# Kernel optimization log

Measured on AMD Instinct MI355X. Metric: run time of the kernel, lower is better.

The kernel has to match this reference:

```python
import jax, jax.numpy as jnp
import numpy as np

H = 16
DH = 64  # n_state // n_head = 1024 // 16
EPS = 1e-6


def phi(x):
    return jax.nn.silu(x) + 1.0


def setup_inputs() -> dict:
    key = jax.random.key(0)
    ks = jax.random.split(key, 9)
    B, C, Tq, Tk = 8, 1024, 1500, 1500
    s = 1.0 / np.sqrt(C).astype(np.float32)
    return {
        "x": jax.random.normal(ks[0], (B, C, Tq, 1), jnp.float32),
        "xa": jax.random.normal(ks[1], (B, C, Tk, 1), jnp.float32),
        "Wq": jax.random.normal(ks[2], (C, C), jnp.float32) * s,
        "bq": jax.random.normal(ks[3], (C,), jnp.float32) * s,
        "Wk": jax.random.normal(ks[4], (C, C), jnp.float32) * s,
        "Wv": jax.random.normal(ks[5], (C, C), jnp.float32) * s,
        "bv": jax.random.normal(ks[6], (C,), jnp.float32) * s,
        "Wo": jax.random.normal(ks[7], (C, C), jnp.float32) * s,
        "bo": jax.random.normal(ks[8], (C,), jnp.float32) * s,
    }


def reference(x, xa, Wq, bq, Wk, Wv, bv, Wo, bo):
    # x: (B,C,Tq,1), xa: (B,C,Tk,1). 1x1 conv2d == matmul over channel dim.
    xq = x[..., 0]   # (B,C,Tq)
    xk = xa[..., 0]  # (B,C,Tk)
    q = jnp.einsum('oc,bct->bot', Wq, xq) + bq[None, :, None]
    k = jnp.einsum('oc,bct->bot', Wk, xk)  # key has no bias
    v = jnp.einsum('oc,bct->bot', Wv, xk) + bv[None, :, None]

    B, C, Tq = q.shape
    Tk = k.shape[2]
    pq = phi(q).reshape(B, H, DH, Tq)
    pk = phi(k).reshape(B, H, DH, Tk)
    vv = v.reshape(B, H, DH, Tk)

    k_sum = pk.sum(axis=3)            # (B,H,Dh) : sum_t phi(k)
    kv_sum = (pk * vv).sum(axis=3)    # (B,H,Dh) : diagonal phi(k)*v sum (as in source)
    den = jnp.einsum('bhdt,bhd->bht', pq, k_sum) + EPS  # (B,H,Tq)

    out = pq * kv_sum[..., None] / den[:, :, None, :]   # (B,H,Dh,Tq)
    out = out.reshape(B, C, Tq) / jnp.sqrt(jnp.asarray(DH, out.dtype))
    y = jnp.einsum('oc,bct->bot', Wo, out) + bo[None, :, None]
    return y[..., None]  # (B,C,Tq,1)
```

## Files before the change

### kernel.cpp

```cpp
#include <hip/hip_runtime.h>

typedef __attribute__((ext_vector_type(4))) float  f32x4;
typedef __attribute__((ext_vector_type(4))) float  float4v;
typedef __attribute__((ext_vector_type(8))) short  short8;
typedef __attribute__((ext_vector_type(4))) short  short4v;

#define TQ 1500
#define TP 1536
#define CC 1024
#define EPS 1e-6f

#define XT_OFF    ((size_t)0)
#define XAT_OFF   ((size_t)25165824)
#define OUT_OFF   ((size_t)50331648)
#define WB_OFF    ((size_t)75497472)
#define KSUM_OFF  ((size_t)83886080)
#define KVSUM_OFF ((size_t)83918848)

#define VMCNT4() asm volatile("s_waitcnt vmcnt(4)" ::: "memory")
#define VMCNT0() asm volatile("s_waitcnt vmcnt(0)" ::: "memory")
#define LGKM0()  asm volatile("s_waitcnt lgkmcnt(0)" ::: "memory")
#define SBAR()   __builtin_amdgcn_s_barrier()
#define SCHED0() __builtin_amdgcn_sched_barrier(0)

__device__ __forceinline__ float bf2f(short s) {
    union { unsigned u; float f; } v; v.u = ((unsigned)(unsigned short)s) << 16; return v.f;
}
__device__ __forceinline__ short f2bf(float f) {
    union { float f; unsigned u; } v; v.f = f;
    unsigned r = (v.u + 0x7FFFu + ((v.u >> 16) & 1u)) >> 16;
    return (short)r;
}
__device__ __forceinline__ float phi_f(float x) {
    return x / (1.f + __expf(-x)) + 1.f;
}
__device__ __forceinline__ void gl_lds16(const void* g, void* l) {
    __builtin_amdgcn_global_load_lds((const __attribute__((address_space(1))) void*)g,
                                     (__attribute__((address_space(3))) void*)l, 16, 0, 0);
}


__global__ __launch_bounds__(256)
void conv_w_kernel(const float* __restrict__ w0, const float* __restrict__ w1,
                   const float* __restrict__ w2, const float* __restrict__ w3,
                   short* __restrict__ o0, short* __restrict__ o1,
                   short* __restrict__ o2, short* __restrict__ o3)
{
    const int i = (blockIdx.x * 256 + threadIdx.x) * 4;
    float4v a = *(const float4v*)(w0 + i);
    float4v b = *(const float4v*)(w1 + i);
    float4v c = *(const float4v*)(w2 + i);
    float4v d = *(const float4v*)(w3 + i);
    short4v ra, rb, rc, rd;
#pragma unroll
    for (int j = 0; j < 4; ++j) {
        ra[j] = f2bf(a[j]); rb[j] = f2bf(b[j]); rc[j] = f2bf(c[j]); rd[j] = f2bf(d[j]);
    }
    *(short4v*)(o0 + i) = ra;
    *(short4v*)(o1 + i) = rb;
    *(short4v*)(o2 + i) = rc;
    *(short4v*)(o3 + i) = rd;
}

__global__ __launch_bounds__(256)
void xpose_kernel(const float* __restrict__ x, const float* __restrict__ xa,
                  short* __restrict__ xT, short* __restrict__ xaT)
{
    __shared__ float tile[64][65];
    const int z  = blockIdx.z;
    const int b  = z & 7;
    const float* src = (z < 8) ? x : xa;
    short* dst       = (z < 8) ? xT : xaT;
    const int c0 = blockIdx.y * 64;
    const int t0 = blockIdx.x * 64;
    const int tl = threadIdx.x & 63;
    const int q  = threadIdx.x >> 6;
    const int t  = t0 + tl;
#pragma unroll
    for (int i = 0; i < 16; ++i) {
        const int cl = q * 16 + i;
        float v = 0.f;
        if (t < TQ) v = src[((size_t)b * CC + c0 + cl) * TQ + t];
        tile[cl][tl] = v;
    }
    __syncthreads();
#pragma unroll
    for (int i = 0; i < 16; ++i) {
        const int t2 = q * 16 + i;
        dst[((size_t)b * TP + t0 + t2) * CC + c0 + tl] = f2bf(tile[tl][t2]);
    }
}


__global__ __launch_bounds__(256, 4)
void gemm_q_out_kernel(const short* __restrict__ xT, const short* __restrict__ Wqb,
                       const float* __restrict__ bq, const float* __restrict__ ksum,
                       const float* __restrict__ kvsum, short* __restrict__ outT)
{
    __shared__ short lds[3][8192];
    const int f    = blockIdx.x;
    const int L    = (f & 7) * 96 + (f >> 3);
    const int nt   = L % 8;
    const int mrow = L / 8;
    const int b    = mrow / 12;
    const int tid  = threadIdx.x;
    const int wave = tid >> 6, lane = tid & 63;
    const int wr = wave >> 1;
    const int wc = wave & 1;
    const int rl = lane & 15;
    const int q4 = lane >> 4;
    const int rg = (q4 ^ ((rl >> 1) & 3)) << 3;

    const int lrow = lane >> 2;
    const int kc   = ((lane & 3) ^ ((lrow >> 1) & 3)) << 3;
    const int row0 = wave * 32 + lrow;
    const short* aP0 = xT  + (size_t)(mrow * 128 + row0) * CC + kc;
    const short* aP1 = aP0 + 16 * CC;
    const short* bP0 = Wqb + (size_t)(nt * 128 + row0) * CC + kc;
    const short* bP1 = bP0 + 16 * CC;
    const int aD0 = wave * 1024, aD1 = aD0 + 512;
    const int bD0 = 4096 + aD0,  bD1 = bD0 + 512;

    const int aoff0 = (wr * 64 + rl) * 32 + rg;
    const int boff0 = 4096 + (wc * 64 + rl) * 32 + rg;

    f32x4 acc[4][4] = {};

#pragma unroll
    for (int s = 0; s < 2; ++s) {
        gl_lds16(aP0, &lds[s][aD0]); gl_lds16(aP1, &lds[s][aD1]);
        gl_lds16(bP0, &lds[s][bD0]); gl_lds16(bP1, &lds[s][bD1]);
        aP0 += 32; aP1 += 32; bP0 += 32; bP1 += 32;
    }
    VMCNT4(); SBAR();

    int cur = 0;
#pragma unroll 1
    for (int kt = 0; kt < 32; ++kt) {
        if (kt <= 29) {
            const int pn = (cur == 0) ? 2 : cur - 1;
            gl_lds16(aP0, &lds[pn][aD0]); gl_lds16(aP1, &lds[pn][aD1]);
            gl_lds16(bP0, &lds[pn][bD0]); gl_lds16(bP1, &lds[pn][bD1]);
            aP0 += 32; aP1 += 32; bP0 += 32; bP1 += 32;
        }
        short8 ra[4], rb[4];
#pragma unroll
        for (int i = 0; i < 4; ++i) {
            ra[i] = *(const short8*)&lds[cur][aoff0 + i * 512];
            rb[i] = *(const short8*)&lds[cur][boff0 + i * 512];
        }
        LGKM0(); SCHED0();
        __builtin_amdgcn_s_setprio(1);
#pragma unroll
        for (int i = 0; i < 4; ++i)
#pragma unroll
            for (int j = 0; j < 4; ++j)
                acc[i][j] = __builtin_amdgcn_mfma_f32_16x16x32_bf16(ra[i], rb[j], acc[i][j], 0, 0, 0);
        __builtin_amdgcn_s_setprio(0);
        if (kt <= 29)      { VMCNT4(); }
        else if (kt == 30) { VMCNT0(); }
        if (kt < 31) SBAR();
        cur = (cur == 2) ? 0 : cur + 1;
    }

    float bias[4], ks[4], kv[4];
#pragma unroll
    for (int j = 0; j < 4; ++j) {
        const int c = nt * 128 + wc * 64 + j * 16 + rl;
        bias[j] = bq[c];
        ks[j]   = ksum[b * CC + c];
        kv[j]   = kvsum[b * CC + c];
    }
#pragma unroll
    for (int i = 0; i < 4; ++i)
#pragma unroll
        for (int j = 0; j < 4; ++j)
#pragma unroll
            for (int r = 0; r < 4; ++r)
                acc[i][j][r] = phi_f(acc[i][j][r] + bias[j]);
#pragma unroll
    for (int i = 0; i < 4; ++i) {
#pragma unroll
        for (int r = 0; r < 4; ++r) {
            float d = acc[i][0][r] * ks[0] + acc[i][1][r] * ks[1]
                    + acc[i][2][r] * ks[2] + acc[i][3][r] * ks[3];
            d += __shfl_xor(d, 1); d += __shfl_xor(d, 2);
            d += __shfl_xor(d, 4); d += __shfl_xor(d, 8);
            const float inv = 0.125f / (d + EPS);
            const int trow = mrow * 128 + wr * 64 + i * 16 + q4 * 4 + r;
#pragma unroll
            for (int j = 0; j < 4; ++j) {
                const int c = nt * 128 + wc * 64 + j * 16 + rl;
                outT[(size_t)trow * CC + c] = f2bf(acc[i][j][r] * kv[j] * inv);
            }
        }
    }
}

__global__ __launch_bounds__(256, 4)
void gemm_kv_kernel(const short* __restrict__ xaT, const short* __restrict__ Wkb,
                    const short* __restrict__ Wvb, const float* __restrict__ bv,
                    float* __restrict__ ksum, float* __restrict__ kvsum)
{
    __shared__ short lds[3][8192];
    const int f    = blockIdx.x;
    const int L    = (f & 7) * 192 + (f >> 3);
    const int cb   = L % 16;
    const int mrow = L / 16;
    const int b    = mrow / 12;
    const int tid  = threadIdx.x;
    const int wave = tid >> 6, lane = tid & 63;
    const int wr = wave >> 1;
    const int wc = wave & 1;
    const int rl = lane & 15;
    const int q4 = lane >> 4;
    const int rg = (q4 ^ ((rl >> 1) & 3)) << 3;

    const int lrow = lane >> 2;
    const int kc   = ((lane & 3) ^ ((lrow >> 1) & 3)) << 3;
    const int row0 = wave * 32 + lrow;
    const short* aP0 = xaT + (size_t)(mrow * 128 + row0) * CC + kc;
    const short* aP1 = aP0 + 16 * CC;
    const short* bPanel = (wave < 2)
        ? Wkb + (size_t)cb * 64 * CC
        : Wvb + (size_t)cb * 64 * CC - (size_t)64 * CC;
    const short* bP0 = bPanel + (size_t)row0 * CC + kc;
    const short* bP1 = bP0 + 16 * CC;
    const int aD0 = wave * 1024, aD1 = aD0 + 512;
    const int bD0 = 4096 + aD0,  bD1 = bD0 + 512;

    const int aoff0 = (wr * 64 + rl) * 32 + rg;
    const int boffK = 4096 + (wc * 32 + rl) * 32 + rg;
    const int boffV = boffK + 2048;

    f32x4 acc[4][4] = {};

#pragma unroll
    for (int s = 0; s < 2; ++s) {
        gl_lds16(aP0, &lds[s][aD0]); gl_lds16(aP1, &lds[s][aD1]);
        gl_lds16(bP0, &lds[s][bD0]); gl_lds16(bP1, &lds[s][bD1]);
        aP0 += 32; aP1 += 32; bP0 += 32; bP1 += 32;
    }
    VMCNT4(); SBAR();

    int cur = 0;
#pragma unroll 1
    for (int kt = 0; kt < 32; ++kt) {
        if (kt <= 29) {
            const int pn = (cur == 0) ? 2 : cur - 1;
            gl_lds16(aP0, &lds[pn][aD0]); gl_lds16(aP1, &lds[pn][aD1]);
            gl_lds16(bP0, &lds[pn][bD0]); gl_lds16(bP1, &lds[pn][bD1]);
            aP0 += 32; aP1 += 32; bP0 += 32; bP1 += 32;
        }
        short8 ra[4], rb[4];
#pragma unroll
        for (int i = 0; i < 4; ++i)
            ra[i] = *(const short8*)&lds[cur][aoff0 + i * 512];
#pragma unroll
        for (int j = 0; j < 2; ++j) {
            rb[j]     = *(const short8*)&lds[cur][boffK + j * 512];
            rb[j + 2] = *(const short8*)&lds[cur][boffV + j * 512];
        }
        LGKM0(); SCHED0();
        __builtin_amdgcn_s_setprio(1);
#pragma unroll
        for (int i = 0; i < 4; ++i)
#pragma unroll
            for (int j = 0; j < 4; ++j)
                acc[i][j] = __builtin_amdgcn_mfma_f32_16x16x32_bf16(ra[i], rb[j], acc[i][j], 0, 0, 0);
        __builtin_amdgcn_s_setprio(0);
        if (kt <= 29)      { VMCNT4(); }
        else if (kt == 30) { VMCNT0(); }
        if (kt < 31) SBAR();
        cur = (cur == 2) ? 0 : cur + 1;
    }

    const int tq0 = (mrow % 12) * 128 + wr * 64 + q4 * 4;
#pragma unroll
    for (int jj = 0; jj < 2; ++jj) {
        const int c = cb * 64 + wc * 32 + jj * 16 + rl;
        const float bvc = bv[c];
        float sk = 0.f, skv = 0.f;
#pragma unroll
        for (int i = 0; i < 4; ++i) {
#pragma unroll
            for (int r = 0; r < 4; ++r) {
                if (tq0 + i * 16 + r < TQ) {
                    float pk = phi_f(acc[i][jj][r]);
                    float vv = acc[i][jj + 2][r] + bvc;
                    sk  += pk;
                    skv += pk * vv;
                }
            }
        }
        sk  += __shfl_xor(sk, 16);  sk  += __shfl_xor(sk, 32);
        skv += __shfl_xor(skv, 16); skv += __shfl_xor(skv, 32);
        if (q4 == 0) {
            atomicAdd(&ksum[b * CC + c], sk);
            atomicAdd(&kvsum[b * CC + c], skv);
        }
    }
}

__global__ __launch_bounds__(256, 4)
void gemm_o_kernel(const short* __restrict__ Wob, const short* __restrict__ outT,
                   const float* __restrict__ bo, float* __restrict__ y)
{
    __shared__ short lds[3][8192];
    const int f    = blockIdx.x;
    const int L    = (f & 7) * 96 + (f >> 3);
    const int ct   = L % 8;
    const int rest = L / 8;
    const int b    = rest / 12;
    const int tt   = rest % 12;
    const int tid  = threadIdx.x;
    const int wave = tid >> 6, lane = tid & 63;
    const int wr = wave >> 1;
    const int wc = wave & 1;
    const int rl = lane & 15;
    const int q4 = lane >> 4;
    const int rg = (q4 ^ ((rl >> 1) & 3)) << 3;

    const int lrow = lane >> 2;
    const int kc   = ((lane & 3) ^ ((lrow >> 1) & 3)) << 3;
    const int row0 = wave * 32 + lrow;
    const short* aP0 = Wob  + (size_t)(ct * 128 + row0) * CC + kc;
    const short* aP1 = aP0 + 16 * CC;
    const short* bP0 = outT + (size_t)(rest * 128 + row0) * CC + kc;
    const short* bP1 = bP0 + 16 * CC;
    const int aD0 = wave * 1024, aD1 = aD0 + 512;
    const int bD0 = 4096 + aD0,  bD1 = bD0 + 512;

    const int aoff0 = (wr * 64 + rl) * 32 + rg;
    const int boff0 = 4096 + (wc * 64 + rl) * 32 + rg;

    f32x4 acc[4][4] = {};

#pragma unroll
    for (int s = 0; s < 2; ++s) {
        gl_lds16(aP0, &lds[s][aD0]); gl_lds16(aP1, &lds[s][aD1]);
        gl_lds16(bP0, &lds[s][bD0]); gl_lds16(bP1, &lds[s][bD1]);
        aP0 += 32; aP1 += 32; bP0 += 32; bP1 += 32;
    }
    VMCNT4(); SBAR();

    int cur = 0;
#pragma unroll 1
    for (int kt = 0; kt < 32; ++kt) {
        if (kt <= 29) {
            const int pn = (cur == 0) ? 2 : cur - 1;
            gl_lds16(aP0, &lds[pn][aD0]); gl_lds16(aP1, &lds[pn][aD1]);
            gl_lds16(bP0, &lds[pn][bD0]); gl_lds16(bP1, &lds[pn][bD1]);
            aP0 += 32; aP1 += 32; bP0 += 32; bP1 += 32;
        }
        short8 ra[4], rb[4];
#pragma unroll
        for (int i = 0; i < 4; ++i) {
            ra[i] = *(const short8*)&lds[cur][aoff0 + i * 512];
            rb[i] = *(const short8*)&lds[cur][boff0 + i * 512];
        }
        LGKM0(); SCHED0();
        __builtin_amdgcn_s_setprio(1);
#pragma unroll
        for (int i = 0; i < 4; ++i)
#pragma unroll
            for (int j = 0; j < 4; ++j)
                acc[i][j] = __builtin_amdgcn_mfma_f32_16x16x32_bf16(ra[i], rb[j], acc[i][j], 0, 0, 0);
        __builtin_amdgcn_s_setprio(0);
        if (kt <= 29)      { VMCNT4(); }
        else if (kt == 30) { VMCNT0(); }
        if (kt < 31) SBAR();
        cur = (cur == 2) ? 0 : cur + 1;
    }

#pragma unroll
    for (int j = 0; j < 4; ++j) {
        const int t = tt * 128 + wc * 64 + j * 16 + rl;
        if (t >= TQ) continue;
#pragma unroll
        for (int i = 0; i < 4; ++i) {
            const int cbase = ct * 128 + wr * 64 + i * 16 + q4 * 4;
#pragma unroll
            for (int r = 0; r < 4; ++r) {
                const int c = cbase + r;
                y[((size_t)b * CC + c) * TQ + t] = acc[i][j][r] + bo[c];
            }
        }
    }
}

extern "C" void kernel_launch(void* const* d_in, const int* in_sizes, int n_in,
                              void* d_out, int out_size, void* d_ws, size_t ws_size,
                              hipStream_t stream)
{
    (void)in_sizes; (void)n_in; (void)out_size; (void)ws_size;
    const float* x  = (const float*)d_in[0];
    const float* xa = (const float*)d_in[1];
    const float* Wq = (const float*)d_in[2];
    const float* bq = (const float*)d_in[3];
    const float* Wk = (const float*)d_in[4];
    const float* Wv = (const float*)d_in[5];
    const float* bv = (const float*)d_in[6];
    const float* Wo = (const float*)d_in[7];
    const float* bo = (const float*)d_in[8];
    float* y = (float*)d_out;
    char* ws = (char*)d_ws;

    short* xT    = (short*)(ws + XT_OFF);
    short* xaT   = (short*)(ws + XAT_OFF);
    short* outT  = (short*)(ws + OUT_OFF);
    short* Wqb   = (short*)(ws + WB_OFF);
    short* Wkb   = Wqb + (size_t)CC * CC;
    short* Wvb   = Wkb + (size_t)CC * CC;
    short* Wob   = Wvb + (size_t)CC * CC;
    float* ksum  = (float*)(ws + KSUM_OFF);
    float* kvsum = (float*)(ws + KVSUM_OFF);

    conv_w_kernel<<<dim3(CC * CC / 4 / 256), 256, 0, stream>>>(Wq, Wk, Wv, Wo, Wqb, Wkb, Wvb, Wob);
    xpose_kernel<<<dim3(TP / 64, CC / 64, 16), 256, 0, stream>>>(x, xa, xT, xaT);
    hipMemsetAsync(ws + KSUM_OFF, 0, 65536, stream);

    gemm_kv_kernel<<<dim3(1536), 256, 0, stream>>>(xaT, Wkb, Wvb, bv, ksum, kvsum);
    gemm_q_out_kernel<<<dim3(768), 256, 0, stream>>>(xT, Wqb, bq, ksum, kvsum, outT);
    gemm_o_kernel<<<dim3(768), 256, 0, stream>>>(Wob, outT, bo, y);
}
```

Before: 324.8 us.

## Deepen GEMM LDS pipeline to 4 stages with register double-buffering; fuse prep kernels

All three GEMM kernels move from a 3-stage LDS ring to a 4-stage ring with a deeper prologue. The K loop is unrolled by two and double-buffers operand fragments in registers, so LDS reads for the next step overlap the MFMAs of the current one. Occupancy hints drop from 4 to 2 blocks per CU to make room for the extra registers and LDS. Weight conversion, input transposition and zeroing of the ksum/kvsum buffers are merged into one prep kernel, which removes two launches and the memset. The risk is lower occupancy reducing latency hiding.

```diff
diff --git a/kernel.cpp b/kernel.cpp
--- a/kernel.cpp
+++ b/kernel.cpp
@@ -17,9 +17,9 @@
 #define KSUM_OFF  ((size_t)83886080)
 #define KVSUM_OFF ((size_t)83918848)
 
+#define VMCNT8() asm volatile("s_waitcnt vmcnt(8)" ::: "memory")
 #define VMCNT4() asm volatile("s_waitcnt vmcnt(4)" ::: "memory")
 #define VMCNT0() asm volatile("s_waitcnt vmcnt(0)" ::: "memory")
-#define LGKM0()  asm volatile("s_waitcnt lgkmcnt(0)" ::: "memory")
 #define SBAR()   __builtin_amdgcn_s_barrier()
 #define SCHED0() __builtin_amdgcn_sched_barrier(0)
 
@@ -41,63 +41,84 @@
 
 
 __global__ __launch_bounds__(256)
-void conv_w_kernel(const float* __restrict__ w0, const float* __restrict__ w1,
-                   const float* __restrict__ w2, const float* __restrict__ w3,
-                   short* __restrict__ o0, short* __restrict__ o1,
-                   short* __restrict__ o2, short* __restrict__ o3)
-{
-    const int i = (blockIdx.x * 256 + threadIdx.x) * 4;
-    float4v a = *(const float4v*)(w0 + i);
-    float4v b = *(const float4v*)(w1 + i);
-    float4v c = *(const float4v*)(w2 + i);
-    float4v d = *(const float4v*)(w3 + i);
-    short4v ra, rb, rc, rd;
-#pragma unroll
-    for (int j = 0; j < 4; ++j) {
-        ra[j] = f2bf(a[j]); rb[j] = f2bf(b[j]); rc[j] = f2bf(c[j]); rd[j] = f2bf(d[j]);
-    }
-    *(short4v*)(o0 + i) = ra;
-    *(short4v*)(o1 + i) = rb;
-    *(short4v*)(o2 + i) = rc;
-    *(short4v*)(o3 + i) = rd;
-}
-
-__global__ __launch_bounds__(256)
-void xpose_kernel(const float* __restrict__ x, const float* __restrict__ xa,
-                  short* __restrict__ xT, short* __restrict__ xaT)
+void prep_kernel(const float* __restrict__ x, const float* __restrict__ xa,
+                 const float* __restrict__ w0, const float* __restrict__ w1,
+                 const float* __restrict__ w2, const float* __restrict__ w3,
+                 short* __restrict__ o0, short* __restrict__ o1,
+                 short* __restrict__ o2, short* __restrict__ o3,
+                 short* __restrict__ xT, short* __restrict__ xaT,
+                 float* __restrict__ zbuf)
 {
     __shared__ float tile[64][65];
-    const int z  = blockIdx.z;
-    const int b  = z & 7;
-    const float* src = (z < 8) ? x : xa;
-    short* dst       = (z < 8) ? xT : xaT;
-    const int c0 = blockIdx.y * 64;
-    const int t0 = blockIdx.x * 64;
-    const int tl = threadIdx.x & 63;
-    const int q  = threadIdx.x >> 6;
-    const int t  = t0 + tl;
-#pragma unroll
-    for (int i = 0; i < 16; ++i) {
-        const int cl = q * 16 + i;
-        float v = 0.f;
-        if (t < TQ) v = src[((size_t)b * CC + c0 + cl) * TQ + t];
-        tile[cl][tl] = v;
-    }
-    __syncthreads();
-#pragma unroll
-    for (int i = 0; i < 16; ++i) {
-        const int t2 = q * 16 + i;
-        dst[((size_t)b * TP + t0 + t2) * CC + c0 + tl] = f2bf(tile[tl][t2]);
-    }
-}
-
-
-__global__ __launch_bounds__(256, 4)
+    const int bid = blockIdx.x;
+    const int tid = threadIdx.x;
+    if (bid < 1024) {
+        const int i = (bid * 256 + tid) * 4;
+        float4v a = *(const float4v*)(w0 + i);
+        float4v b = *(const float4v*)(w1 + i);
+        float4v c = *(const float4v*)(w2 + i);
+        float4v d = *(const float4v*)(w3 + i);
+        short4v ra, rb, rc, rd;
+#pragma unroll
+        for (int j = 0; j < 4; ++j) {
+            ra[j] = f2bf(a[j]); rb[j] = f2bf(b[j]); rc[j] = f2bf(c[j]); rd[j] = f2bf(d[j]);
+        }
+        *(short4v*)(o0 + i) = ra;
+        *(short4v*)(o1 + i) = rb;
+        *(short4v*)(o2 + i) = rc;
+        *(short4v*)(o3 + i) = rd;
+        if (bid < 16) {
+            const int zb = bid * 1024 + tid;
+            zbuf[zb] = 0.f; zbuf[zb + 256] = 0.f; zbuf[zb + 512] = 0.f; zbuf[zb + 768] = 0.f;
+        }
+    } else {
+        const int idx = bid - 1024;
+        const int t0 = (idx % 24) * 64;
+        const int c0 = ((idx / 24) % 16) * 64;
+        const int z  = idx / 384;
+        const int b  = z & 7;
+        const float* src = (z < 8) ? x : xa;
+        short* dst       = (z < 8) ? xT : xaT;
+        const int tl = tid & 63;
+        const int q  = tid >> 6;
+        const int t  = t0 + tl;
+#pragma unroll
+        for (int i = 0; i < 16; ++i) {
+            const int cl = q * 16 + i;
+            float v = 0.f;
+            if (t < TQ) v = src[((size_t)b * CC + c0 + cl) * TQ + t];
+            tile[cl][tl] = v;
+        }
+        __syncthreads();
+#pragma unroll
+        for (int i = 0; i < 16; ++i) {
+            const int t2 = q * 16 + i;
+            dst[((size_t)b * TP + t0 + t2) * CC + c0 + tl] = f2bf(tile[tl][t2]);
+        }
+    }
+}
+
+
+#define GEMM_PROLOGUE()                                                         \
+    for (int s = 0; s < 3; ++s) {                                               \
+        gl_lds16(aP0, &lds[s][aD0]); gl_lds16(aP1, &lds[s][aD1]);               \
+        gl_lds16(bP0, &lds[s][bD0]); gl_lds16(bP1, &lds[s][bD1]);               \
+        aP0 += 32; aP1 += 32; bP0 += 32; bP1 += 32;                             \
+    }                                                                           \
+    VMCNT8(); SBAR();
+
+#define STAGE_NEXT(buf)                                                         \
+    { short* lb = &lds[buf][0];                                                 \
+      gl_lds16(aP0, lb + aD0); gl_lds16(aP1, lb + aD1);                         \
+      gl_lds16(bP0, lb + bD0); gl_lds16(bP1, lb + bD1);                         \
+      aP0 += 32; aP1 += 32; bP0 += 32; bP1 += 32; }
+
+__global__ __launch_bounds__(256, 2)
 void gemm_q_out_kernel(const short* __restrict__ xT, const short* __restrict__ Wqb,
                        const float* __restrict__ bq, const float* __restrict__ ksum,
                        const float* __restrict__ kvsum, short* __restrict__ outT)
 {
-    __shared__ short lds[3][8192];
+    __shared__ short lds[4][8192];
     const int f    = blockIdx.x;
     const int L    = (f & 7) * 96 + (f >> 3);
     const int nt   = L % 8;
@@ -125,42 +146,54 @@
     const int boff0 = 4096 + (wc * 64 + rl) * 32 + rg;
 
     f32x4 acc[4][4] = {};
-
-#pragma unroll
-    for (int s = 0; s < 2; ++s) {
-        gl_lds16(aP0, &lds[s][aD0]); gl_lds16(aP1, &lds[s][aD1]);
-        gl_lds16(bP0, &lds[s][bD0]); gl_lds16(bP1, &lds[s][bD1]);
-        aP0 += 32; aP1 += 32; bP0 += 32; bP1 += 32;
-    }
-    VMCNT4(); SBAR();
-
-    int cur = 0;
+    short8 a0[4], b0[4], a1[4], b1[4];
+
+    GEMM_PROLOGUE();
+    { const short* bp = &lds[0][0];
+#pragma unroll
+      for (int i = 0; i < 4; ++i) {
+          a0[i] = *(const short8*)(bp + aoff0 + i * 512);
+          b0[i] = *(const short8*)(bp + boff0 + i * 512);
+      } }
+
 #pragma unroll 1
-    for (int kt = 0; kt < 32; ++kt) {
-        if (kt <= 29) {
-            const int pn = (cur == 0) ? 2 : cur - 1;
-            gl_lds16(aP0, &lds[pn][aD0]); gl_lds16(aP1, &lds[pn][aD1]);
-            gl_lds16(bP0, &lds[pn][bD0]); gl_lds16(bP1, &lds[pn][bD1]);
-            aP0 += 32; aP1 += 32; bP0 += 32; bP1 += 32;
-        }
-        short8 ra[4], rb[4];
-#pragma unroll
-        for (int i = 0; i < 4; ++i) {
-            ra[i] = *(const short8*)&lds[cur][aoff0 + i * 512];
-            rb[i] = *(const short8*)&lds[cur][boff0 + i * 512];
-        }
-        LGKM0(); SCHED0();
-        __builtin_amdgcn_s_setprio(1);
-#pragma unroll
-        for (int i = 0; i < 4; ++i)
-#pragma unroll
-            for (int j = 0; j < 4; ++j)
-                acc[i][j] = __builtin_amdgcn_mfma_f32_16x16x32_bf16(ra[i], rb[j], acc[i][j], 0, 0, 0);
-        __builtin_amdgcn_s_setprio(0);
-        if (kt <= 29)      { VMCNT4(); }
-        else if (kt == 30) { VMCNT0(); }
-        if (kt < 31) SBAR();
-        cur = (cur == 2) ? 0 : cur + 1;
+    for (int it = 0; it < 16; ++it) {
+        const int ks0 = it * 2;
+        if (ks0 == 30) { VMCNT0(); } else { VMCNT4(); }
+        SBAR();
+        { const short* bp = &lds[(ks0 + 1) & 3][0];
+#pragma unroll
+          for (int i = 0; i < 4; ++i) {
+              a1[i] = *(const short8*)(bp + aoff0 + i * 512);
+              b1[i] = *(const short8*)(bp + boff0 + i * 512);
+          } }
+        if (it < 15) STAGE_NEXT((ks0 + 3) & 3);
+        SCHED0();
+        __builtin_amdgcn_s_setprio(1);
+#pragma unroll
+        for (int i = 0; i < 4; ++i)
+#pragma unroll
+            for (int j = 0; j < 4; ++j)
+                acc[i][j] = __builtin_amdgcn_mfma_f32_16x16x32_bf16(a0[i], b0[j], acc[i][j], 0, 0, 0);
+        __builtin_amdgcn_s_setprio(0);
+        if (it < 15) {
+            VMCNT4(); SBAR();
+            { const short* bp = &lds[(ks0 + 2) & 3][0];
+#pragma unroll
+              for (int i = 0; i < 4; ++i) {
+                  a0[i] = *(const short8*)(bp + aoff0 + i * 512);
+                  b0[i] = *(const short8*)(bp + boff0 + i * 512);
+              } }
+            if (it < 14) STAGE_NEXT((ks0 + 4) & 3);
+            SCHED0();
+        }
+        __builtin_amdgcn_s_setprio(1);
+#pragma unroll
+        for (int i = 0; i < 4; ++i)
+#pragma unroll
+            for (int j = 0; j < 4; ++j)
+                acc[i][j] = __builtin_amdgcn_mfma_f32_16x16x32_bf16(a1[i], b1[j], acc[i][j], 0, 0, 0);
+        __builtin_amdgcn_s_setprio(0);
     }
 
     float bias[4], ks[4], kv[4];
@@ -197,12 +230,12 @@
     }
 }
 
-__global__ __launch_bounds__(256, 4)
+__global__ __launch_bounds__(256, 2)
 void gemm_kv_kernel(const short* __restrict__ xaT, const short* __restrict__ Wkb,
                     const short* __restrict__ Wvb, const float* __restrict__ bv,
                     float* __restrict__ ksum, float* __restrict__ kvsum)
 {
-    __shared__ short lds[3][8192];
+    __shared__ short lds[4][8192];
     const int f    = blockIdx.x;
     const int L    = (f & 7) * 192 + (f >> 3);
     const int cb   = L % 16;
@@ -234,45 +267,63 @@
     const int boffV = boffK + 2048;
 
     f32x4 acc[4][4] = {};
-
-#pragma unroll
-    for (int s = 0; s < 2; ++s) {
-        gl_lds16(aP0, &lds[s][aD0]); gl_lds16(aP1, &lds[s][aD1]);
-        gl_lds16(bP0, &lds[s][bD0]); gl_lds16(bP1, &lds[s][bD1]);
-        aP0 += 32; aP1 += 32; bP0 += 32; bP1 += 32;
-    }
-    VMCNT4(); SBAR();
-
-    int cur = 0;
+    short8 a0[4], b0[4], a1[4], b1[4];
+
+    GEMM_PROLOGUE();
+    { const short* bp = &lds[0][0];
+#pragma unroll
+      for (int i = 0; i < 4; ++i)
+          a0[i] = *(const short8*)(bp + aoff0 + i * 512);
+#pragma unroll
+      for (int j = 0; j < 2; ++j) {
+          b0[j]     = *(const short8*)(bp + boffK + j * 512);
+          b0[j + 2] = *(const short8*)(bp + boffV + j * 512);
+      } }
+
 #pragma unroll 1
-    for (int kt = 0; kt < 32; ++kt) {
-        if (kt <= 29) {
-            const int pn = (cur == 0) ? 2 : cur - 1;
-            gl_lds16(aP0, &lds[pn][aD0]); gl_lds16(aP1, &lds[pn][aD1]);
-            gl_lds16(bP0, &lds[pn][bD0]); gl_lds16(bP1, &lds[pn][bD1]);
-            aP0 += 32; aP1 += 32; bP0 += 32; bP1 += 32;
-        }
-        short8 ra[4], rb[4];
-#pragma unroll
-        for (int i = 0; i < 4; ++i)
-            ra[i] = *(const short8*)&lds[cur][aoff0 + i * 512];
-#pragma unroll
-        for (int j = 0; j < 2; ++j) {
-            rb[j]     = *(const short8*)&lds[cur][boffK + j * 512];
-            rb[j + 2] = *(const short8*)&lds[cur][boffV + j * 512];
-        }
-        LGKM0(); SCHED0();
-        __builtin_amdgcn_s_setprio(1);
-#pragma unroll
-        for (int i = 0; i < 4; ++i)
-#pragma unroll
-            for (int j = 0; j < 4; ++j)
-                acc[i][j] = __builtin_amdgcn_mfma_f32_16x16x32_bf16(ra[i], rb[j], acc[i][j], 0, 0, 0);
-        __builtin_amdgcn_s_setprio(0);
-        if (kt <= 29)      { VMCNT4(); }
-        else if (kt == 30) { VMCNT0(); }
-        if (kt < 31) SBAR();
-        cur = (cur == 2) ? 0 : cur + 1;
+    for (int it = 0; it < 16; ++it) {
+        const int ks0 = it * 2;
+        if (ks0 == 30) { VMCNT0(); } else { VMCNT4(); }
+        SBAR();
+        { const short* bp = &lds[(ks0 + 1) & 3][0];
+#pragma unroll
+          for (int i = 0; i < 4; ++i)
+              a1[i] = *(const short8*)(bp + aoff0 + i * 512);
+#pragma unroll
+          for (int j = 0; j < 2; ++j) {
+              b1[j]     = *(const short8*)(bp + boffK + j * 512);
+              b1[j + 2] = *(const short8*)(bp + boffV + j * 512);
+          } }
+        if (it < 15) STAGE_NEXT((ks0 + 3) & 3);
+        SCHED0();
+        __builtin_amdgcn_s_setprio(1);
+#pragma unroll
+        for (int i = 0; i < 4; ++i)
+#pragma unroll
+            for (int j = 0; j < 4; ++j)
+                acc[i][j] = __builtin_amdgcn_mfma_f32_16x16x32_bf16(a0[i], b0[j], acc[i][j], 0, 0, 0);
+        __builtin_amdgcn_s_setprio(0);
+        if (it < 15) {
+            VMCNT4(); SBAR();
+            { const short* bp = &lds[(ks0 + 2) & 3][0];
+#pragma unroll
+              for (int i = 0; i < 4; ++i)
+                  a0[i] = *(const short8*)(bp + aoff0 + i * 512);
+#pragma unroll
+              for (int j = 0; j < 2; ++j) {
+                  b0[j]     = *(const short8*)(bp + boffK + j * 512);
+                  b0[j + 2] = *(const short8*)(bp + boffV + j * 512);
+              } }
+            if (it < 14) STAGE_NEXT((ks0 + 4) & 3);
+            SCHED0();
+        }
+        __builtin_amdgcn_s_setprio(1);
+#pragma unroll
+        for (int i = 0; i < 4; ++i)
+#pragma unroll
+            for (int j = 0; j < 4; ++j)
+                acc[i][j] = __builtin_amdgcn_mfma_f32_16x16x32_bf16(a1[i], b1[j], acc[i][j], 0, 0, 0);
+        __builtin_amdgcn_s_setprio(0);
     }
 
     const int tq0 = (mrow % 12) * 128 + wr * 64 + q4 * 4;
@@ -302,11 +353,11 @@
     }
 }
 
-__global__ __launch_bounds__(256, 4)
+__global__ __launch_bounds__(256, 2)
 void gemm_o_kernel(const short* __restrict__ Wob, const short* __restrict__ outT,
                    const float* __restrict__ bo, float* __restrict__ y)
 {
-    __shared__ short lds[3][8192];
+    __shared__ short lds[4][8192];
     const int f    = blockIdx.x;
     const int L    = (f & 7) * 96 + (f >> 3);
     const int ct   = L % 8;
@@ -335,42 +386,54 @@
     const int boff0 = 4096 + (wc * 64 + rl) * 32 + rg;
 
     f32x4 acc[4][4] = {};
-
-#pragma unroll
-    for (int s = 0; s < 2; ++s) {
-        gl_lds16(aP0, &lds[s][aD0]); gl_lds16(aP1, &lds[s][aD1]);
-        gl_lds16(bP0, &lds[s][bD0]); gl_lds16(bP1, &lds[s][bD1]);
-        aP0 += 32; aP1 += 32; bP0 += 32; bP1 += 32;
-    }
-    VMCNT4(); SBAR();
-
-    int cur = 0;
+    short8 a0[4], b0[4], a1[4], b1[4];
+
+    GEMM_PROLOGUE();
+    { const short* bp = &lds[0][0];
+#pragma unroll
+      for (int i = 0; i < 4; ++i) {
+          a0[i] = *(const short8*)(bp + aoff0 + i * 512);
+          b0[i] = *(const short8*)(bp + boff0 + i * 512);
+      } }
+
 #pragma unroll 1
-    for (int kt = 0; kt < 32; ++kt) {
-        if (kt <= 29) {
-            const int pn = (cur == 0) ? 2 : cur - 1;
-            gl_lds16(aP0, &lds[pn][aD0]); gl_lds16(aP1, &lds[pn][aD1]);
-            gl_lds16(bP0, &lds[pn][bD0]); gl_lds16(bP1, &lds[pn][bD1]);
-            aP0 += 32; aP1 += 32; bP0 += 32; bP1 += 32;
-        }
-        short8 ra[4], rb[4];
-#pragma unroll
-        for (int i = 0; i < 4; ++i) {
-            ra[i] = *(const short8*)&lds[cur][aoff0 + i * 512];
-            rb[i] = *(const short8*)&lds[cur][boff0 + i * 512];
-        }
-        LGKM0(); SCHED0();
-        __builtin_amdgcn_s_setprio(1);
-#pragma unroll
-        for (int i = 0; i < 4; ++i)
-#pragma unroll
-            for (int j = 0; j < 4; ++j)
-                acc[i][j] = __builtin_amdgcn_mfma_f32_16x16x32_bf16(ra[i], rb[j], acc[i][j], 0, 0, 0);
-        __builtin_amdgcn_s_setprio(0);
-        if (kt <= 29)      { VMCNT4(); }
-        else if (kt == 30) { VMCNT0(); }
-        if (kt < 31) SBAR();
-        cur = (cur == 2) ? 0 : cur + 1;
+    for (int it = 0; it < 16; ++it) {
+        const int ks0 = it * 2;
+        if (ks0 == 30) { VMCNT0(); } else { VMCNT4(); }
+        SBAR();
+        { const short* bp = &lds[(ks0 + 1) & 3][0];
+#pragma unroll
+          for (int i = 0; i < 4; ++i) {
+              a1[i] = *(const short8*)(bp + aoff0 + i * 512);
+              b1[i] = *(const short8*)(bp + boff0 + i * 512);
+          } }
+        if (it < 15) STAGE_NEXT((ks0 + 3) & 3);
+        SCHED0();
+        __builtin_amdgcn_s_setprio(1);
+#pragma unroll
+        for (int i = 0; i < 4; ++i)
+#pragma unroll
+            for (int j = 0; j < 4; ++j)
+                acc[i][j] = __builtin_amdgcn_mfma_f32_16x16x32_bf16(a0[i], b0[j], acc[i][j], 0, 0, 0);
+        __builtin_amdgcn_s_setprio(0);
+        if (it < 15) {
+            VMCNT4(); SBAR();
+            { const short* bp = &lds[(ks0 + 2) & 3][0];
+#pragma unroll
+              for (int i = 0; i < 4; ++i) {
+                  a0[i] = *(const short8*)(bp + aoff0 + i * 512);
+                  b0[i] = *(const short8*)(bp + boff0 + i * 512);
+              } }
+            if (it < 14) STAGE_NEXT((ks0 + 4) & 3);
+            SCHED0();
+        }
+        __builtin_amdgcn_s_setprio(1);
+#pragma unroll
+        for (int i = 0; i < 4; ++i)
+#pragma unroll
+            for (int j = 0; j < 4; ++j)
+                acc[i][j] = __builtin_amdgcn_mfma_f32_16x16x32_bf16(a1[i], b1[j], acc[i][j], 0, 0, 0);
+        __builtin_amdgcn_s_setprio(0);
     }
 
 #pragma unroll
@@ -416,10 +479,8 @@
     float* ksum  = (float*)(ws + KSUM_OFF);
     float* kvsum = (float*)(ws + KVSUM_OFF);
 
-    conv_w_kernel<<<dim3(CC * CC / 4 / 256), 256, 0, stream>>>(Wq, Wk, Wv, Wo, Wqb, Wkb, Wvb, Wob);
-    xpose_kernel<<<dim3(TP / 64, CC / 64, 16), 256, 0, stream>>>(x, xa, xT, xaT);
-    hipMemsetAsync(ws + KSUM_OFF, 0, 65536, stream);
-
+    prep_kernel<<<dim3(1024 + 6144), 256, 0, stream>>>(x, xa, Wq, Wk, Wv, Wo,
+                                                       Wqb, Wkb, Wvb, Wob, xT, xaT, ksum);
     gemm_kv_kernel<<<dim3(1536), 256, 0, stream>>>(xaT, Wkb, Wvb, bv, ksum, kvsum);
     gemm_q_out_kernel<<<dim3(768), 256, 0, stream>>>(xT, Wqb, bq, ksum, kvsum, outT);
     gemm_o_kernel<<<dim3(768), 256, 0, stream>>>(Wob, outT, bo, y);
```

Measured after the change: 311.2 us. -4.2%, faster.
